# Optimization experiments

Hardware: AMD Instinct MI355X
Metric: run time of the kernel (lower is better)

The kernel has to match this reference:

```python
import jax, jax.numpy as jnp
import numpy as np

N_NODES = 40000
N_EDGES = 640000
D = 128


def setup_inputs() -> dict:
    key = jax.random.key(0)
    k1, k2, k3, k4, k5 = jax.random.split(key, 5)
    x = jax.random.normal(k1, (N_NODES, D), dtype=jnp.float32)
    edge_index = jax.random.randint(k2, (2, N_EDGES), 0, N_NODES, dtype=jnp.int64)
    # torch Linear stores weight as [out, in]; xavier ~ scaled normal
    scale = (2.0 / (D + D)) ** 0.5
    W_self = jax.random.normal(k3, (D, D), dtype=jnp.float32) * scale
    W_neigh = jax.random.normal(k4, (D, D), dtype=jnp.float32) * scale
    bias = jax.random.normal(k5, (D,), dtype=jnp.float32) * 0.01
    return {"x": x, "edge_index": edge_index, "W_self": W_self,
            "W_neigh": W_neigh, "bias": bias}


def reference(x, edge_index, W_self, W_neigh, bias):
    num_nodes = x.shape[0]
    row, col = edge_index[0], edge_index[1]
    # gather source features and scatter-add into destination nodes
    agg = jax.ops.segment_sum(x[row], col, num_segments=num_nodes)  # [N, D]
    deg = jax.ops.segment_sum(jnp.ones_like(col, dtype=x.dtype), col,
                              num_segments=num_nodes)
    agg = agg / jnp.clip(deg, 1.0)[:, None]
    # h_v = lin_self(x_v) + lin_neigh(mean_u x_u) + bias  (no activation in source)
    out = x @ W_self.T + agg @ W_neigh.T + bias
    return out
```

## Files before the change

kernel.cpp:

```cpp
#include <hip/hip_runtime.h>

#define N_NODES 40000
#define N_EDGES 640000
#define D 128
#define KCAT 256
#define CAP 64

typedef __attribute__((ext_vector_type(8))) short short8v;
typedef __attribute__((ext_vector_type(4))) float f32x4;
typedef __attribute__((ext_vector_type(2))) float f32x2;


__device__ inline unsigned short f2bf(float f) {
  union { float f; unsigned int u; } v{f};
  unsigned int r = (v.u + 0x7FFFu + ((v.u >> 16) & 1u)) >> 16;
  return (unsigned short)r;
}

__global__ __launch_bounds__(256) void prep_count_kernel(
    const float* __restrict__ x, const float* __restrict__ Ws,
    const float* __restrict__ Wn, const int* __restrict__ ei, char* outb,
    unsigned short* __restrict__ Wcat, unsigned int* __restrict__ x8,
    int* __restrict__ deg, int* __restrict__ slot) {
  int tid = blockIdx.x * 256 + threadIdx.x;
  {
    int node = tid >> 5;
    int l = tid & 31;
    float4 v = *reinterpret_cast<const float4*>(x + (size_t)node * D + l * 4);
    ushort4 h;
    h.x = f2bf(v.x); h.y = f2bf(v.y); h.z = f2bf(v.z); h.w = f2bf(v.w);
    *reinterpret_cast<ushort4*>(outb + (size_t)node * 512 + l * 8) = h;
    unsigned int u = __builtin_amdgcn_cvt_pk_fp8_f32(v.x, v.y, 0, false);
    u = __builtin_amdgcn_cvt_pk_fp8_f32(v.z, v.w, u, true);
    x8[tid] = u;
  }
  if (tid < 8192) {
    int j = tid >> 6;
    int kq = tid & 63;
    int k0 = kq * 4;
    float4 v = (kq < 32)
        ? *reinterpret_cast<const float4*>(Ws + j * D + k0)
        : *reinterpret_cast<const float4*>(Wn + j * D + (k0 - D));
    ushort4 h;
    h.x = f2bf(v.x); h.y = f2bf(v.y); h.z = f2bf(v.z); h.w = f2bf(v.w);
    *reinterpret_cast<ushort4*>(Wcat + j * KCAT + k0) = h;
  }
  if (tid < N_EDGES / 4) {
    int4 r = *reinterpret_cast<const int4*>(ei + tid * 4);
    int4 c = *reinterpret_cast<const int4*>(ei + N_EDGES + tid * 4);
    slot[c.x * CAP + atomicAdd(&deg[c.x], 1)] = r.x;
    slot[c.y * CAP + atomicAdd(&deg[c.y], 1)] = r.y;
    slot[c.z * CAP + atomicAdd(&deg[c.z], 1)] = r.z;
    slot[c.w * CAP + atomicAdd(&deg[c.w], 1)] = r.w;
  }
}

__global__ __launch_bounds__(256) void gather_kernel(
    const unsigned int* __restrict__ x8, char* outb,
    const int* __restrict__ deg, const int* __restrict__ slot) {
  int node = blockIdx.x * 8 + (threadIdx.x >> 5);
  int l = threadIdx.x & 31;
  int nd = deg[node];
  const int* sp = slot + (size_t)node * CAP;
  float a0 = 0.f, a1 = 0.f, a2 = 0.f, a3 = 0.f;
  int e = 0;
  for (; e + 8 <= nd; e += 8) {
    unsigned int v[8];
#pragma unroll
    for (int j = 0; j < 8; ++j) v[j] = x8[(size_t)sp[e + j] * 32 + l];
#pragma unroll
    for (int j = 0; j < 8; ++j) {
      f32x2 lo = __builtin_amdgcn_cvt_pk_f32_fp8(v[j], false);
      f32x2 hi = __builtin_amdgcn_cvt_pk_f32_fp8(v[j], true);
      a0 += lo.x; a1 += lo.y; a2 += hi.x; a3 += hi.y;
    }
  }
  for (; e + 4 <= nd; e += 4) {
    unsigned int v[4];
#pragma unroll
    for (int j = 0; j < 4; ++j) v[j] = x8[(size_t)sp[e + j] * 32 + l];
#pragma unroll
    for (int j = 0; j < 4; ++j) {
      f32x2 lo = __builtin_amdgcn_cvt_pk_f32_fp8(v[j], false);
      f32x2 hi = __builtin_amdgcn_cvt_pk_f32_fp8(v[j], true);
      a0 += lo.x; a1 += lo.y; a2 += hi.x; a3 += hi.y;
    }
  }
  for (; e < nd; ++e) {
    unsigned int v = x8[(size_t)sp[e] * 32 + l];
    f32x2 lo = __builtin_amdgcn_cvt_pk_f32_fp8(v, false);
    f32x2 hi = __builtin_amdgcn_cvt_pk_f32_fp8(v, true);
    a0 += lo.x; a1 += lo.y; a2 += hi.x; a3 += hi.y;
  }
  float inv = 1.0f / fmaxf((float)nd, 1.0f);
  ushort4 h;
  h.x = f2bf(a0 * inv); h.y = f2bf(a1 * inv);
  h.z = f2bf(a2 * inv); h.w = f2bf(a3 * inv);
  *reinterpret_cast<ushort4*>(outb + (size_t)node * 512 + 256 + l * 8) = h;
}

__global__ __launch_bounds__(256) void sage_gemm_kernel(
    const char* ab, const unsigned short* __restrict__ Wcat,
    const float* __restrict__ bias, float* out) {
  __shared__ __align__(16) char Abuf[64 * 512];
  const int t = threadIdx.x;
  const int wave = t >> 6;
  const int lane = t & 63;
  const int node0 = blockIdx.x * 64;

  short8v breg[2][8];
#pragma unroll
  for (int jg = 0; jg < 2; ++jg) {
    int col = wave * 32 + jg * 16 + (lane & 15);
#pragma unroll
    for (int ks = 0; ks < 8; ++ks) {
      int k0 = ks * 32 + (lane >> 4) * 8;
      breg[jg][ks] =
          *reinterpret_cast<const short8v*>(Wcat + (size_t)col * KCAT + k0);
    }
  }

#pragma unroll
  for (int i = 0; i < 8; ++i) {
    int sl = i * 256 + t;
    int row = sl >> 5;
    int s = sl & 31;
    int4 v = *reinterpret_cast<const int4*>(
        ab + (size_t)(node0 + row) * 512 + s * 16);
    *reinterpret_cast<int4*>(Abuf + row * 512 + ((s ^ (row & 7)) << 4)) = v;
  }
  __syncthreads();

  const int srow = lane & 15;
  const int c7 = lane & 7;
  const int sb = lane >> 4;

  f32x4 acc[4][2] = {};
#pragma unroll
  for (int ks = 0; ks < 8; ++ks) {
    short8v af[4];
#pragma unroll
    for (int mf = 0; mf < 4; ++mf) {
      int row = mf * 16 + srow;
      int sl = (ks * 4 + sb) ^ c7;
      af[mf] = *reinterpret_cast<const short8v*>(Abuf + row * 512 + (sl << 4));
    }
#pragma unroll
    for (int mf = 0; mf < 4; ++mf)
#pragma unroll
      for (int jg = 0; jg < 2; ++jg)
        acc[mf][jg] = __builtin_amdgcn_mfma_f32_16x16x32_bf16(
            af[mf], breg[jg][ks], acc[mf][jg], 0, 0, 0);
  }
  __syncthreads();

#pragma unroll
  for (int jg = 0; jg < 2; ++jg) {
    int col = wave * 32 + jg * 16 + (lane & 15);
    float bv = bias[col];
#pragma unroll
    for (int mf = 0; mf < 4; ++mf) {
      int rbase = node0 + mf * 16 + (lane >> 4) * 4;
#pragma unroll
      for (int r = 0; r < 4; ++r) {
        out[(size_t)(rbase + r) * D + col] = acc[mf][jg][r] + bv;
      }
    }
  }
}

extern "C" void kernel_launch(void* const* d_in, const int* in_sizes, int n_in,
                              void* d_out, int out_size, void* d_ws, size_t ws_size,
                              hipStream_t stream) {
  const float* x    = (const float*)d_in[0];
  const int*   ei   = (const int*)d_in[1];
  const float* Ws   = (const float*)d_in[2];
  const float* Wn   = (const float*)d_in[3];
  const float* bias = (const float*)d_in[4];
  float* out = (float*)d_out;
  char* outb = (char*)d_out;

  unsigned short* Wcat = (unsigned short*)d_ws;
  int* deg  = (int*)(Wcat + 128 * KCAT);
  int* slot = deg + N_NODES;
  unsigned int* x8 = (unsigned int*)(slot + (size_t)N_NODES * CAP);

  hipMemsetAsync(deg, 0, N_NODES * sizeof(int), stream);
  prep_count_kernel<<<5000, 256, 0, stream>>>(x, Ws, Wn, ei, outb, Wcat, x8,
                                              deg, slot);
  gather_kernel<<<5000, 256, 0, stream>>>(x8, outb, deg, slot);
  sage_gemm_kernel<<<625, 256, 0, stream>>>(outb, Wcat, bias, out);
}
```

Measured before the change: 85.53 us.

## Partition edge bucketing by XCD and store neighbor slots as 16-bit

Edge bucketing now uses 1000 blocks. Each block scans one chunk of edges but only inserts edges whose destination falls in the node range assigned to its XCD (block index mod 8). The aim is to keep the degree atomics and slot writes inside one XCD's L2 instead of bouncing lines across dies. Neighbor slot indices are stored as unsigned short, which halves slot traffic in both the bucketing and gather kernels; this is valid because the 40000 nodes fit in 16 bits. In exchange, every edge index is read eight times, and the work depends on the hardware dispatching blocks round-robin across XCDs.

```diff
diff --git a/kernel.cpp b/kernel.cpp
--- a/kernel.cpp
+++ b/kernel.cpp
@@ -5,6 +5,10 @@
 #define D 128
 #define KCAT 256
 #define CAP 64
+#define NXCD 8
+#define PART 5000
+#define BUCKET_BLOCKS 1000
+#define CHUNK_I4 1280
 
 typedef __attribute__((ext_vector_type(8))) short short8v;
 typedef __attribute__((ext_vector_type(4))) float f32x4;
@@ -21,8 +25,10 @@
     const float* __restrict__ x, const float* __restrict__ Ws,
     const float* __restrict__ Wn, const int* __restrict__ ei, char* outb,
     unsigned short* __restrict__ Wcat, unsigned int* __restrict__ x8,
-    int* __restrict__ deg, int* __restrict__ slot) {
-  int tid = blockIdx.x * 256 + threadIdx.x;
+    int* __restrict__ deg, unsigned short* __restrict__ slot) {
+  int b = blockIdx.x;
+  int t = threadIdx.x;
+  int tid = b * 256 + t;
   {
     int node = tid >> 5;
     int l = tid & 31;
@@ -45,23 +51,37 @@
     h.x = f2bf(v.x); h.y = f2bf(v.y); h.z = f2bf(v.z); h.w = f2bf(v.w);
     *reinterpret_cast<ushort4*>(Wcat + j * KCAT + k0) = h;
   }
-  if (tid < N_EDGES / 4) {
-    int4 r = *reinterpret_cast<const int4*>(ei + tid * 4);
-    int4 c = *reinterpret_cast<const int4*>(ei + N_EDGES + tid * 4);
-    slot[c.x * CAP + atomicAdd(&deg[c.x], 1)] = r.x;
-    slot[c.y * CAP + atomicAdd(&deg[c.y], 1)] = r.y;
-    slot[c.z * CAP + atomicAdd(&deg[c.z], 1)] = r.z;
-    slot[c.w * CAP + atomicAdd(&deg[c.w], 1)] = r.w;
+  if (b < BUCKET_BLOCKS) {
+    int p = b & (NXCD - 1);
+    int chunk = b >> 3;
+    int lo = p * PART;
+    const int4* rq = reinterpret_cast<const int4*>(ei) + chunk * CHUNK_I4;
+    const int4* cq =
+        reinterpret_cast<const int4*>(ei + N_EDGES) + chunk * CHUNK_I4;
+#pragma unroll
+    for (int j = 0; j < 5; ++j) {
+      int q = j * 256 + t;
+      int4 r = rq[q];
+      int4 c = cq[q];
+      if ((unsigned)(c.x - lo) < PART)
+        slot[(size_t)c.x * CAP + atomicAdd(&deg[c.x], 1)] = (unsigned short)r.x;
+      if ((unsigned)(c.y - lo) < PART)
+        slot[(size_t)c.y * CAP + atomicAdd(&deg[c.y], 1)] = (unsigned short)r.y;
+      if ((unsigned)(c.z - lo) < PART)
+        slot[(size_t)c.z * CAP + atomicAdd(&deg[c.z], 1)] = (unsigned short)r.z;
+      if ((unsigned)(c.w - lo) < PART)
+        slot[(size_t)c.w * CAP + atomicAdd(&deg[c.w], 1)] = (unsigned short)r.w;
+    }
   }
 }
 
 __global__ __launch_bounds__(256) void gather_kernel(
     const unsigned int* __restrict__ x8, char* outb,
-    const int* __restrict__ deg, const int* __restrict__ slot) {
+    const int* __restrict__ deg, const unsigned short* __restrict__ slot) {
   int node = blockIdx.x * 8 + (threadIdx.x >> 5);
   int l = threadIdx.x & 31;
   int nd = deg[node];
-  const int* sp = slot + (size_t)node * CAP;
+  const unsigned short* sp = slot + (size_t)node * CAP;
   float a0 = 0.f, a1 = 0.f, a2 = 0.f, a3 = 0.f;
   int e = 0;
   for (; e + 8 <= nd; e += 8) {
@@ -181,9 +201,10 @@
   char* outb = (char*)d_out;
 
   unsigned short* Wcat = (unsigned short*)d_ws;
-  int* deg  = (int*)(Wcat + 128 * KCAT);
-  int* slot = deg + N_NODES;
-  unsigned int* x8 = (unsigned int*)(slot + (size_t)N_NODES * CAP);
+  int* deg = (int*)(Wcat + 128 * KCAT);
+  unsigned short* slot = (unsigned short*)(deg + N_NODES);
+  unsigned int* x8 =
+      (unsigned int*)(slot + (size_t)N_NODES * CAP);
 
   hipMemsetAsync(deg, 0, N_NODES * sizeof(int), stream);
   prep_count_kernel<<<5000, 256, 0, stream>>>(x, Ws, Wn, ei, outb, Wcat, x8,
```

Measured after the change: 70.24 us, median of 2. 17.9% less time.
